# Optimization experiments

Hardware: AMD Instinct MI355X
Metric: run time of the kernel (lower is better)

The kernel has to match this reference:

```python
import jax, jax.numpy as jnp
import numpy as np

N = 50000
E = 800000
IN_C, HID, OUT_C = 128, 128, 40
EPS = 1e-5  # BatchNorm eps


def setup_inputs() -> dict:
    key = jax.random.key(0)
    ks = jax.random.split(key, 8)
    x = jax.random.normal(ks[0], (N, IN_C), dtype=jnp.float32)
    edge_index = jax.random.randint(ks[1], (2, E), 0, N, dtype=jnp.int64)
    s1 = 1.0 / np.sqrt(IN_C)
    s2 = 1.0 / np.sqrt(HID)
    return {
        "x": x,
        "edge_index": edge_index,
        "W1": jax.random.uniform(ks[2], (IN_C, HID), jnp.float32, -s1, s1),
        "b1": jnp.zeros((HID,), jnp.float32),
        "g1": jnp.ones((HID,), jnp.float32),
        "beta1": jnp.zeros((HID,), jnp.float32),
        "W2": jax.random.uniform(ks[3], (HID, HID), jnp.float32, -s2, s2),
        "b2": jnp.zeros((HID,), jnp.float32),
        "g2": jnp.ones((HID,), jnp.float32),
        "beta2": jnp.zeros((HID,), jnp.float32),
        "W3": jax.random.uniform(ks[4], (HID, OUT_C), jnp.float32, -s2, s2),
        "b3": jnp.zeros((OUT_C,), jnp.float32),
    }


def _gcn_norm(src, dst, num_nodes):
    # symmetric normalization D^-1/2 A D^-1/2, no self loops, unit edge weights
    deg = jax.ops.segment_sum(jnp.ones_like(dst, dtype=jnp.float32), dst,
                              num_segments=num_nodes)
    dinv = jnp.where(deg > 0, jax.lax.rsqrt(jnp.maximum(deg, 1.0)), 0.0)
    return dinv[src] * dinv[dst]  # [E]


def _conv(h, W, b, src, dst, norm, num_nodes):
    h = h @ W  # linear transform first (fewer message features)
    msg = norm[:, None] * h[src]  # [E, F] gather
    out = jax.ops.segment_sum(msg, dst, num_segments=num_nodes)  # scatter-add
    return out + b


def _bn_relu(h, g, beta):
    mu = jnp.mean(h, axis=0)
    var = jnp.mean(jnp.square(h - mu), axis=0)  # biased, as torch BN
    hn = (h - mu) * jax.lax.rsqrt(var + EPS) * g + beta
    return jax.nn.relu(hn)


def reference(x, edge_index, W1, b1, g1, beta1, W2, b2, g2, beta2, W3, b3):
    src, dst = edge_index[0], edge_index[1]
    norm = _gcn_norm(src, dst, N)  # cached=True: shared across layers
    h = _bn_relu(_conv(x, W1, b1, src, dst, norm, N), g1, beta1)
    h = _bn_relu(_conv(h, W2, b2, src, dst, norm, N), g2, beta2)
    return _conv(h, W3, b3, src, dst, norm, N)
```

## Files before the change

kernel.cpp:

```cpp
#include <hip/hip_runtime.h>
#include <hip/hip_fp16.h>

typedef _Float16 half8 __attribute__((ext_vector_type(8)));
typedef float floatx4 __attribute__((ext_vector_type(4)));


__device__ __forceinline__ void unpack8(uint4 v, float* f) {
    const __half2* hp = (const __half2*)&v;
    float2 a = __half22float2(hp[0]);
    float2 b = __half22float2(hp[1]);
    float2 c = __half22float2(hp[2]);
    float2 d = __half22float2(hp[3]);
    f[0] = a.x; f[1] = a.y; f[2] = b.x; f[3] = b.y;
    f[4] = c.x; f[5] = c.y; f[6] = d.x; f[7] = d.y;
}

__device__ __forceinline__ uint4 pack8(const float* f) {
    __half2 h0 = __floats2half2_rn(f[0], f[1]);
    __half2 h1 = __floats2half2_rn(f[2], f[3]);
    __half2 h2 = __floats2half2_rn(f[4], f[5]);
    __half2 h3 = __floats2half2_rn(f[6], f[7]);
    uint4 v;
    v.x = *(const unsigned int*)&h0;
    v.y = *(const unsigned int*)&h1;
    v.z = *(const unsigned int*)&h2;
    v.w = *(const unsigned int*)&h3;
    return v;
}


__global__ void k_setup(const float* __restrict__ W1, const float* __restrict__ W2,
                        const float* __restrict__ W3, __half* __restrict__ Wt1,
                        __half* __restrict__ Wt2, __half* __restrict__ Wt3,
                        int* __restrict__ zp, int zn) {
    const int PW = 2 * 128 * 128 + 48 * 128;
    int i = blockIdx.x * 256 + threadIdx.x;
    if (i < 128 * 128) {
        int n = i >> 7, k = i & 127;
        Wt1[i] = __float2half(W1[(size_t)k * 128 + n]);
    } else if (i < 2 * 128 * 128) {
        int j = i - 128 * 128;
        int n = j >> 7, k = j & 127;
        Wt2[j] = __float2half(W2[(size_t)k * 128 + n]);
    } else if (i < PW) {
        int j = i - 2 * 128 * 128;
        int n = j >> 7, k = j & 127;
        Wt3[j] = (n < 40) ? __float2half(W3[(size_t)k * 40 + n]) : __half(0.f);
    } else {
        int j = i - PW;
        if (j < zn) zp[j] = 0;
    }
}


__global__ void k_deg_xcd(const int* __restrict__ dst, int* __restrict__ deg,
                          int E, int rs) {
    int lo = (blockIdx.x & 7) * rs;
    int i = (blockIdx.x >> 3) * 256 + threadIdx.x;
    if (i < E) {
        int d = dst[i];
        if (d >= lo && d < lo + rs) atomicAdd(&deg[d], 1);
    }
}

__global__ void k_place_xcd(const int* __restrict__ src, const int* __restrict__ dst,
                            int* __restrict__ cursor, unsigned short* __restrict__ sidx,
                            int E, int rs) {
    int lo = (blockIdx.x & 7) * rs;
    int i = (blockIdx.x >> 3) * 256 + threadIdx.x;
    if (i < E) {
        int d = dst[i];
        if (d >= lo && d < lo + rs) {
            int pos = atomicAdd(&cursor[d], 1);
            sidx[pos] = (unsigned short)src[i];
        }
    }
}

__global__ __launch_bounds__(256) void k_chunkscan(const int* __restrict__ deg,
                                                   int* __restrict__ bsum, int n) {
    __shared__ int ls[256];
    int t = threadIdx.x;
    int s = 0;
    int base = t * 256;
    for (int k = 0; k < 256; ++k) {
        int idx = base + k;
        if (idx < n) s += deg[idx];
    }
    ls[t] = s;
    __syncthreads();
    for (int off = 1; off < 256; off <<= 1) {
        int v = t >= off ? ls[t - off] : 0;
        __syncthreads();
        ls[t] += v;
        __syncthreads();
    }
    bsum[t] = ls[t] - s;
}

__global__ void k_scanchunk(const int* __restrict__ cnt, const int* __restrict__ bsum,
                            int* __restrict__ row_ptr, int* __restrict__ cursor,
                            float* __restrict__ dinv, int n, int E) {
    __shared__ int ls[256];
    int i = blockIdx.x * 256 + threadIdx.x;
    int v = i < n ? cnt[i] : 0;
    ls[threadIdx.x] = v;
    __syncthreads();
    for (int off = 1; off < 256; off <<= 1) {
        int t = threadIdx.x >= off ? ls[threadIdx.x - off] : 0;
        __syncthreads();
        ls[threadIdx.x] += t;
        __syncthreads();
    }
    if (i < n) {
        int ex = ls[threadIdx.x] - v + bsum[blockIdx.x];
        row_ptr[i] = ex;
        cursor[i] = ex;
        dinv[i] = v > 0 ? rsqrtf((float)v) : 0.f;
    }
    if (i == n - 1) row_ptr[n] = E;
}


template <int CT, int STRIDE, int VALID, int AMODE, int CSPLIT>
__global__ __launch_bounds__(256) void k_gemm_mfma(const void* __restrict__ Ap,
                                                   const __half* __restrict__ Wt,
                                                   const float* __restrict__ sums32,
                                                   const float* __restrict__ sumsq32,
                                                   const float* __restrict__ g,
                                                   const float* __restrict__ beta,
                                                   const float* __restrict__ dinv,
                                                   __half* __restrict__ C, int nrows) {
    constexpr int CW = CT * 16;
    __shared__ char lw[CT * 16 * 256];
    __shared__ float lsc[128], lsh[128];
    const int rowblk = (CSPLIT == 2) ? (blockIdx.x >> 1) : blockIdx.x;
    const int colblk = (CSPLIT == 2) ? (blockIdx.x & 1) : 0;

    const int lane = threadIdx.x & 63;
    const int wid = threadIdx.x >> 6;
    const int l15 = lane & 15;
    const int lg = lane >> 4;
    const int rowbase = rowblk * 128 + wid * 32;

    uint4 raw16[2][4];
    float4 raw32[2][4][2];
#pragma unroll
    for (int r = 0; r < 2; ++r) {
        int row = rowbase + r * 16 + l15;
        bool ok = row < nrows;
#pragma unroll
        for (int kk = 0; kk < 4; ++kk) {
            const int c0 = kk * 32 + lg * 8;
            if (AMODE == 0) {
                const float* a = (const float*)Ap + (size_t)row * 128 + c0;
                raw32[r][kk][0] = ok ? *(const float4*)a : make_float4(0.f, 0.f, 0.f, 0.f);
                raw32[r][kk][1] = ok ? *(const float4*)(a + 4) : make_float4(0.f, 0.f, 0.f, 0.f);
            } else {
                raw16[r][kk] = ok ? *(const uint4*)((const __half*)Ap + (size_t)row * 128 + c0)
                                  : make_uint4(0, 0, 0, 0);
            }
        }
    }

    const int nu4 = CT * 16 * 16;
    for (int i = threadIdx.x; i < nu4; i += 256) {
        int row = i >> 4, k8 = i & 15;
        uint4 v = ((const uint4*)Wt)[(colblk * CW + row) * 16 + k8];
        *(uint4*)(lw + ((row * 256 + k8 * 16) ^ ((row & 7) << 4))) = v;
    }
    if (AMODE == 1 && threadIdx.x < 128) {
        int c = threadIdx.x;
        float s = 0.f, q = 0.f;
        for (int k2 = 0; k2 < 32; ++k2) {
            s += sums32[k2 * 128 + c];
            q += sumsq32[k2 * 128 + c];
        }
        float inv_n = 1.f / (float)nrows;
        float mu = s * inv_n;
        float var = q * inv_n - mu * mu;
        float rs = rsqrtf(var + 1e-5f);
        float sc = rs * g[c];
        lsc[c] = sc;
        lsh[c] = beta[c] - mu * sc;
    }
    __syncthreads();

    half8 a2[2][4];
#pragma unroll
    for (int r = 0; r < 2; ++r) {
#pragma unroll
        for (int kk = 0; kk < 4; ++kk) {
            const int c0 = kk * 32 + lg * 8;
            half8 h;
            if (AMODE == 0) {
                float4 v0 = raw32[r][kk][0];
                float4 v1 = raw32[r][kk][1];
                h[0] = (_Float16)v0.x; h[1] = (_Float16)v0.y;
                h[2] = (_Float16)v0.z; h[3] = (_Float16)v0.w;
                h[4] = (_Float16)v1.x; h[5] = (_Float16)v1.y;
                h[6] = (_Float16)v1.z; h[7] = (_Float16)v1.w;
            } else {
                float f[8];
                unpack8(raw16[r][kk], f);
                float4 s0 = *(const float4*)&lsc[c0];
                float4 s1 = *(const float4*)&lsc[c0 + 4];
                float4 t0 = *(const float4*)&lsh[c0];
                float4 t1 = *(const float4*)&lsh[c0 + 4];
                h[0] = (_Float16)fmaxf(f[0] * s0.x + t0.x, 0.f);
                h[1] = (_Float16)fmaxf(f[1] * s0.y + t0.y, 0.f);
                h[2] = (_Float16)fmaxf(f[2] * s0.z + t0.z, 0.f);
                h[3] = (_Float16)fmaxf(f[3] * s0.w + t0.w, 0.f);
                h[4] = (_Float16)fmaxf(f[4] * s1.x + t1.x, 0.f);
                h[5] = (_Float16)fmaxf(f[5] * s1.y + t1.y, 0.f);
                h[6] = (_Float16)fmaxf(f[6] * s1.z + t1.z, 0.f);
                h[7] = (_Float16)fmaxf(f[7] * s1.w + t1.w, 0.f);
            }
            a2[r][kk] = h;
        }
    }

    floatx4 acc[2][CT];
#pragma unroll
    for (int r = 0; r < 2; ++r)
#pragma unroll
        for (int c = 0; c < CT; ++c) acc[r][c] = (floatx4){0.f, 0.f, 0.f, 0.f};

#pragma unroll
    for (int kk = 0; kk < 4; ++kk) {
#pragma unroll
        for (int c = 0; c < CT; ++c) {
            int wrow = c * 16 + l15;
            half8 bfrag = *(const half8*)(lw + ((wrow * 256 + kk * 64 + lg * 16) ^ ((wrow & 7) << 4)));
#pragma unroll
            for (int r = 0; r < 2; ++r)
                acc[r][c] = __builtin_amdgcn_mfma_f32_16x16x32_f16(a2[r][kk], bfrag, acc[r][c], 0, 0, 0);
        }
    }

    const int BV = (VALID - colblk * CW) < CW ? (VALID - colblk * CW) : CW;
    __syncthreads();
    __half* ct = (__half*)lw;
#pragma unroll
    for (int r = 0; r < 2; ++r) {
        int lr0 = wid * 32 + r * 16 + lg * 4;
        float d4[4];
#pragma unroll
        for (int j = 0; j < 4; ++j) {
            int row = rowblk * 128 + lr0 + j;
            d4[j] = row < nrows ? dinv[row] : 0.f;
        }
#pragma unroll
        for (int c = 0; c < CT; ++c) {
            int col = c * 16 + l15;
#pragma unroll
            for (int j = 0; j < 4; ++j) {
                int lrow = lr0 + j;
                int cc = (CW == 64) ? (col ^ (((lrow >> 2) & 1) << 5)) : col;
                ct[lrow * CW + cc] = __float2half(acc[r][c][j] * d4[j]);
            }
        }
    }
    __syncthreads();
    constexpr int U = CW / 8;
    for (int i = threadIdx.x; i < 128 * U; i += 256) {
        int lrow = i / U, u = i % U;
        int row = rowblk * 128 + lrow;
        int col0 = u * 8;
        if (row < nrows && col0 < BV) {
            int cc = (CW == 64) ? (col0 ^ (((lrow >> 2) & 1) << 5)) : col0;
            uint4 v = *(const uint4*)&ct[lrow * CW + cc];
            *(uint4*)(&C[(size_t)row * STRIDE + colblk * CW + col0]) = v;
        }
    }
}


__global__ __launch_bounds__(256) void k_agg128_stats(const __half* __restrict__ M,
                                                      const int* __restrict__ rp,
                                                      const unsigned short* __restrict__ sidx,
                                                      const float* __restrict__ dinv,
                                                      __half* __restrict__ Hout,
                                                      float* __restrict__ sums32,
                                                      float* __restrict__ sumsq32, int n) {
    int d = blockIdx.x * 16 + (threadIdx.x >> 4);
    int lane = threadIdx.x & 15;
    float acc[8] = {0.f, 0.f, 0.f, 0.f, 0.f, 0.f, 0.f, 0.f};
    if (d < n) {
        int beg = rp[d], end = rp[d + 1];
        int j = beg;
        for (; j + 8 <= end; j += 8) {
            uint4 v[8];
#pragma unroll
            for (int t = 0; t < 8; ++t)
                v[t] = *(const uint4*)(M + (size_t)sidx[j + t] * 128 + lane * 8);
#pragma unroll
            for (int t = 0; t < 8; ++t) {
                float f[8];
                unpack8(v[t], f);
#pragma unroll
                for (int i = 0; i < 8; ++i) acc[i] += f[i];
            }
        }
        for (; j + 4 <= end; j += 4) {
            uint4 v[4];
#pragma unroll
            for (int t = 0; t < 4; ++t)
                v[t] = *(const uint4*)(M + (size_t)sidx[j + t] * 128 + lane * 8);
#pragma unroll
            for (int t = 0; t < 4; ++t) {
                float f[8];
                unpack8(v[t], f);
#pragma unroll
                for (int i = 0; i < 8; ++i) acc[i] += f[i];
            }
        }
        for (; j < end; ++j) {
            uint4 v = *(const uint4*)(M + (size_t)sidx[j] * 128 + lane * 8);
            float f[8];
            unpack8(v, f);
#pragma unroll
            for (int i = 0; i < 8; ++i) acc[i] += f[i];
        }
        float sc = dinv[d];
#pragma unroll
        for (int i = 0; i < 8; ++i) acc[i] *= sc;
        *(uint4*)(Hout + (size_t)d * 128 + lane * 8) = pack8(acc);
    }
    float sq[8];
#pragma unroll
    for (int i = 0; i < 8; ++i) sq[i] = acc[i] * acc[i];
#pragma unroll
    for (int m = 16; m <= 32; m <<= 1) {
#pragma unroll
        for (int i = 0; i < 8; ++i) {
            acc[i] += __shfl_xor(acc[i], m);
            sq[i]  += __shfl_xor(sq[i], m);
        }
    }
    __shared__ float lsw[2][4][16][8];
    int wid = threadIdx.x >> 6, wl = threadIdx.x & 63;
    if (wl < 16) {
#pragma unroll
        for (int i = 0; i < 8; ++i) {
            lsw[0][wid][wl][i] = acc[i];
            lsw[1][wid][wl][i] = sq[i];
        }
    }
    __syncthreads();
    if (threadIdx.x < 128) {
        int c = threadIdx.x;
        int lc = c >> 3, e = c & 7;
        float ss = 0.f, qq = 0.f;
#pragma unroll
        for (int w = 0; w < 4; ++w) {
            ss += lsw[0][w][lc][e];
            qq += lsw[1][w][lc][e];
        }
        int sh = (blockIdx.x & 31) * 128;
        atomicAdd(&sums32[sh + c], ss);
        atomicAdd(&sumsq32[sh + c], qq);
    }
}


__global__ void k_agg40_f16(const __half* __restrict__ M,
                            const int* __restrict__ rp,
                            const unsigned short* __restrict__ sidx,
                            const float* __restrict__ dinv,
                            const float* __restrict__ b3,
                            float* __restrict__ out, int n) {
    int i = blockIdx.x * 256 + threadIdx.x;
    if (i >= n * 5) return;
    int d = i / 5, q = i % 5;
    int beg = rp[d], end = rp[d + 1];
    float acc[8] = {0.f, 0.f, 0.f, 0.f, 0.f, 0.f, 0.f, 0.f};
    int j = beg;
    for (; j + 4 <= end; j += 4) {
        uint4 v0 = *(const uint4*)(M + (size_t)sidx[j] * 64 + q * 8);
        uint4 v1 = *(const uint4*)(M + (size_t)sidx[j + 1] * 64 + q * 8);
        uint4 v2 = *(const uint4*)(M + (size_t)sidx[j + 2] * 64 + q * 8);
        uint4 v3 = *(const uint4*)(M + (size_t)sidx[j + 3] * 64 + q * 8);
        float f0[8], f1[8], f2[8], f3[8];
        unpack8(v0, f0); unpack8(v1, f1); unpack8(v2, f2); unpack8(v3, f3);
#pragma unroll
        for (int k = 0; k < 8; ++k)
            acc[k] += (f0[k] + f1[k]) + (f2[k] + f3[k]);
    }
    for (; j < end; ++j) {
        uint4 v = *(const uint4*)(M + (size_t)sidx[j] * 64 + q * 8);
        float f[8];
        unpack8(v, f);
#pragma unroll
        for (int k = 0; k < 8; ++k) acc[k] += f[k];
    }
    float sc = dinv[d];
    float4 b0 = *(const float4*)&b3[q * 8];
    float4 b1 = *(const float4*)&b3[q * 8 + 4];
    float4 r0, r1;
    r0.x = acc[0] * sc + b0.x; r0.y = acc[1] * sc + b0.y;
    r0.z = acc[2] * sc + b0.z; r0.w = acc[3] * sc + b0.w;
    r1.x = acc[4] * sc + b1.x; r1.y = acc[5] * sc + b1.y;
    r1.z = acc[6] * sc + b1.z; r1.w = acc[7] * sc + b1.w;
    float* o = out + (size_t)d * 40 + q * 8;
    *(float4*)o = r0;
    *(float4*)(o + 4) = r1;
}


extern "C" void kernel_launch(void* const* d_in, const int* in_sizes, int n_in,
                              void* d_out, int out_size, void* d_ws, size_t ws_size,
                              hipStream_t stream) {
    const float* x  = (const float*)d_in[0];
    const int*   ei = (const int*)d_in[1];
    const float* W1 = (const float*)d_in[2];
    const float* g1 = (const float*)d_in[4];
    const float* be1= (const float*)d_in[5];
    const float* W2 = (const float*)d_in[6];
    const float* g2 = (const float*)d_in[8];
    const float* be2= (const float*)d_in[9];
    const float* W3 = (const float*)d_in[10];
    const float* b3 = (const float*)d_in[11];

    const int N = in_sizes[0] / 128;
    const int E = in_sizes[1] / 2;
    const int* srcv = ei;
    const int* dstv = ei + E;
    const int NB = (N + 255) / 256;
    const int RS = (N + 7) / 8;
    const int EB8 = 8 * ((E + 255) / 256);

    __half* M    = (__half*)d_ws;
    __half* Hb   = M + (size_t)N * 128;
    __half* t3   = Hb + (size_t)N * 128;
    __half* Wt1  = t3 + (size_t)N * 64;
    __half* Wt2  = Wt1 + 128 * 128;
    __half* Wt3  = Wt2 + 128 * 128;
    float* dinv    = (float*)(Wt3 + 48 * 128);
    int*   deg     = (int*)(dinv + N);
    float* sumsA   = (float*)(deg + N);
    float* sumsqA  = sumsA + 32 * 128;
    float* sumsB   = sumsqA + 32 * 128;
    float* sumsqB  = sumsB + 32 * 128;
    int*   row_ptr = (int*)(sumsqB + 32 * 128);
    int*   cursor  = row_ptr + N + 1;
    unsigned short* sidx = (unsigned short*)(cursor + N);
    int*   bsum    = (int*)(sidx + E);
    float* out     = (float*)d_out;

    const int GB = (N + 127) / 128;
    const int ZN = N + 4 * 32 * 128;
    const int SETUP_TOT = 2 * 128 * 128 + 48 * 128 + ZN;

    k_setup<<<(SETUP_TOT + 255) / 256, 256, 0, stream>>>(W1, W2, W3, Wt1, Wt2, Wt3, deg, ZN);
    k_deg_xcd<<<EB8, 256, 0, stream>>>(dstv, deg, E, RS);
    k_chunkscan<<<1, 256, 0, stream>>>(deg, bsum, N);
    k_scanchunk<<<NB, 256, 0, stream>>>(deg, bsum, row_ptr, cursor, dinv, N, E);
    k_place_xcd<<<EB8, 256, 0, stream>>>(srcv, dstv, cursor, sidx, E, RS);

    k_gemm_mfma<4, 128, 128, 0, 2><<<GB * 2, 256, 0, stream>>>(x, Wt1, nullptr, nullptr, nullptr, nullptr, dinv, M, N);
    k_agg128_stats<<<(N + 15) / 16, 256, 0, stream>>>(M, row_ptr, sidx, dinv, Hb, sumsA, sumsqA, N);

    k_gemm_mfma<4, 128, 128, 1, 2><<<GB * 2, 256, 0, stream>>>(Hb, Wt2, sumsA, sumsqA, g1, be1, dinv, M, N);
    k_agg128_stats<<<(N + 15) / 16, 256, 0, stream>>>(M, row_ptr, sidx, dinv, Hb, sumsB, sumsqB, N);

    k_gemm_mfma<3, 64, 40, 1, 1><<<GB, 256, 0, stream>>>(Hb, Wt3, sumsB, sumsqB, g2, be2, dinv, t3, N);
    k_agg40_f16<<<(N * 5 + 255) / 256, 256, 0, stream>>>(t3, row_ptr, sidx, dinv, b3, out, N);
}
```

Baseline: 229.1 us.

## Stripe feature matrices into 32-column slabs and aggregate per slab for cache locality

GEMM outputs and aggregation inputs now use a striped layout: four slabs of N×32 halves instead of row-major N×128. Aggregation runs one 32-column pass per block, with blocks interleaved so each XCD's L2 holds a smaller gather working set. Edge indices are also pre-converted to 16-bit in the setup kernel, which reduces index traffic in the degree and placement kernels. The cost is more blocks and more index reads per aggregation, plus an extra conversion pass over all edges.

```diff
diff --git a/kernel.cpp b/kernel.cpp
--- a/kernel.cpp
+++ b/kernel.cpp
@@ -32,7 +32,9 @@
 __global__ void k_setup(const float* __restrict__ W1, const float* __restrict__ W2,
                         const float* __restrict__ W3, __half* __restrict__ Wt1,
                         __half* __restrict__ Wt2, __half* __restrict__ Wt3,
-                        int* __restrict__ zp, int zn) {
+                        int* __restrict__ zp, int zn,
+                        const int* __restrict__ ei, unsigned short* __restrict__ e16,
+                        int E) {
     const int PW = 2 * 128 * 128 + 48 * 128;
     int i = blockIdx.x * 256 + threadIdx.x;
     if (i < 128 * 128) {
@@ -46,14 +48,17 @@
         int j = i - 2 * 128 * 128;
         int n = j >> 7, k = j & 127;
         Wt3[j] = (n < 40) ? __float2half(W3[(size_t)k * 40 + n]) : __half(0.f);
+    } else if (i < PW + zn) {
+        zp[i - PW] = 0;
     } else {
-        int j = i - PW;
-        if (j < zn) zp[j] = 0;
-    }
-}
-
-
-__global__ void k_deg_xcd(const int* __restrict__ dst, int* __restrict__ deg,
+        int j = i - PW - zn;
+        if (j < E) e16[j] = (unsigned short)ei[E + j];
+        else if (j < 2 * E) e16[j] = (unsigned short)ei[j - E];
+    }
+}
+
+
+__global__ void k_deg_xcd(const unsigned short* __restrict__ dst, int* __restrict__ deg,
                           int E, int rs) {
     int lo = (blockIdx.x & 7) * rs;
     int i = (blockIdx.x >> 3) * 256 + threadIdx.x;
@@ -63,7 +68,8 @@
     }
 }
 
-__global__ void k_place_xcd(const int* __restrict__ src, const int* __restrict__ dst,
+__global__ void k_place_xcd(const unsigned short* __restrict__ src,
+                            const unsigned short* __restrict__ dst,
                             int* __restrict__ cursor, unsigned short* __restrict__ sidx,
                             int E, int rs) {
     int lo = (blockIdx.x & 7) * rs;
@@ -72,7 +78,7 @@
         int d = dst[i];
         if (d >= lo && d < lo + rs) {
             int pos = atomicAdd(&cursor[d], 1);
-            sidx[pos] = (unsigned short)src[i];
+            sidx[pos] = src[i];
         }
     }
 }
@@ -122,7 +128,7 @@
 }
 
 
-template <int CT, int STRIDE, int VALID, int AMODE, int CSPLIT>
+template <int CT, int STRIDE, int VALID, int AMODE, int CSPLIT, int ASTRIPE, int CSTRIPE>
 __global__ __launch_bounds__(256) void k_gemm_mfma(const void* __restrict__ Ap,
                                                    const __half* __restrict__ Wt,
                                                    const float* __restrict__ sums32,
@@ -156,6 +162,9 @@
                 const float* a = (const float*)Ap + (size_t)row * 128 + c0;
                 raw32[r][kk][0] = ok ? *(const float4*)a : make_float4(0.f, 0.f, 0.f, 0.f);
                 raw32[r][kk][1] = ok ? *(const float4*)(a + 4) : make_float4(0.f, 0.f, 0.f, 0.f);
+            } else if (ASTRIPE) {
+                const __half* a = (const __half*)Ap + ((size_t)kk * nrows + row) * 32 + lg * 8;
+                raw16[r][kk] = ok ? *(const uint4*)a : make_uint4(0, 0, 0, 0);
             } else {
                 raw16[r][kk] = ok ? *(const uint4*)((const __half*)Ap + (size_t)row * 128 + c0)
                                   : make_uint4(0, 0, 0, 0);
@@ -238,7 +247,6 @@
         }
     }
 
-    const int BV = (VALID - colblk * CW) < CW ? (VALID - colblk * CW) : CW;
     __syncthreads();
     __half* ct = (__half*)lw;
 #pragma unroll
@@ -267,56 +275,51 @@
         int lrow = i / U, u = i % U;
         int row = rowblk * 128 + lrow;
         int col0 = u * 8;
-        if (row < nrows && col0 < BV) {
+        int g2 = colblk * CW + col0;
+        if (row < nrows && (CSTRIPE || col0 < VALID)) {
             int cc = (CW == 64) ? (col0 ^ (((lrow >> 2) & 1) << 5)) : col0;
             uint4 v = *(const uint4*)&ct[lrow * CW + cc];
-            *(uint4*)(&C[(size_t)row * STRIDE + colblk * CW + col0]) = v;
-        }
-    }
-}
-
-
-__global__ __launch_bounds__(256) void k_agg128_stats(const __half* __restrict__ M,
-                                                      const int* __restrict__ rp,
-                                                      const unsigned short* __restrict__ sidx,
-                                                      const float* __restrict__ dinv,
-                                                      __half* __restrict__ Hout,
-                                                      float* __restrict__ sums32,
-                                                      float* __restrict__ sumsq32, int n) {
-    int d = blockIdx.x * 16 + (threadIdx.x >> 4);
-    int lane = threadIdx.x & 15;
+            if (CSTRIPE)
+                *(uint4*)(&C[((size_t)(g2 >> 5) * nrows + row) * 32 + (g2 & 31)]) = v;
+            else
+                *(uint4*)(&C[(size_t)row * STRIDE + g2]) = v;
+        }
+    }
+}
+
+
+__global__ __launch_bounds__(256) void k_agg32_stats(const __half* __restrict__ M4,
+                                                     const int* __restrict__ rp,
+                                                     const unsigned short* __restrict__ sidx,
+                                                     const float* __restrict__ dinv,
+                                                     __half* __restrict__ H4,
+                                                     float* __restrict__ sums32,
+                                                     float* __restrict__ sumsq32, int n) {
+    int b = blockIdx.x;
+    int pass = (b >> 1) & 3;
+    int nodeblk = (b >> 3) * 2 + (b & 1);
+    int tid = threadIdx.x;
+    int d = nodeblk * 64 + (tid >> 2);
+    int lane4 = tid & 3;
+    const __half* Mp = M4 + (size_t)pass * n * 32;
+
     float acc[8] = {0.f, 0.f, 0.f, 0.f, 0.f, 0.f, 0.f, 0.f};
     if (d < n) {
         int beg = rp[d], end = rp[d + 1];
         int j = beg;
-        for (; j + 8 <= end; j += 8) {
-            uint4 v[8];
-#pragma unroll
-            for (int t = 0; t < 8; ++t)
-                v[t] = *(const uint4*)(M + (size_t)sidx[j + t] * 128 + lane * 8);
-#pragma unroll
-            for (int t = 0; t < 8; ++t) {
-                float f[8];
-                unpack8(v[t], f);
-#pragma unroll
-                for (int i = 0; i < 8; ++i) acc[i] += f[i];
-            }
-        }
         for (; j + 4 <= end; j += 4) {
-            uint4 v[4];
-#pragma unroll
-            for (int t = 0; t < 4; ++t)
-                v[t] = *(const uint4*)(M + (size_t)sidx[j + t] * 128 + lane * 8);
-#pragma unroll
-            for (int t = 0; t < 4; ++t) {
-                float f[8];
-                unpack8(v[t], f);
-#pragma unroll
-                for (int i = 0; i < 8; ++i) acc[i] += f[i];
-            }
+            uint4 v0 = *(const uint4*)(Mp + (size_t)sidx[j]     * 32 + lane4 * 8);
+            uint4 v1 = *(const uint4*)(Mp + (size_t)sidx[j + 1] * 32 + lane4 * 8);
+            uint4 v2 = *(const uint4*)(Mp + (size_t)sidx[j + 2] * 32 + lane4 * 8);
+            uint4 v3 = *(const uint4*)(Mp + (size_t)sidx[j + 3] * 32 + lane4 * 8);
+            float f0[8], f1[8], f2[8], f3[8];
+            unpack8(v0, f0); unpack8(v1, f1); unpack8(v2, f2); unpack8(v3, f3);
+#pragma unroll
+            for (int i = 0; i < 8; ++i)
+                acc[i] += (f0[i] + f1[i]) + (f2[i] + f3[i]);
         }
         for (; j < end; ++j) {
-            uint4 v = *(const uint4*)(M + (size_t)sidx[j] * 128 + lane * 8);
+            uint4 v = *(const uint4*)(Mp + (size_t)sidx[j] * 32 + lane4 * 8);
             float f[8];
             unpack8(v, f);
 #pragma unroll
@@ -325,22 +328,23 @@
         float sc = dinv[d];
 #pragma unroll
         for (int i = 0; i < 8; ++i) acc[i] *= sc;
-        *(uint4*)(Hout + (size_t)d * 128 + lane * 8) = pack8(acc);
-    }
+        *(uint4*)(H4 + (size_t)pass * n * 32 + (size_t)d * 32 + lane4 * 8) = pack8(acc);
+    }
+
     float sq[8];
 #pragma unroll
     for (int i = 0; i < 8; ++i) sq[i] = acc[i] * acc[i];
 #pragma unroll
-    for (int m = 16; m <= 32; m <<= 1) {
+    for (int m = 4; m <= 32; m <<= 1) {
 #pragma unroll
         for (int i = 0; i < 8; ++i) {
             acc[i] += __shfl_xor(acc[i], m);
             sq[i]  += __shfl_xor(sq[i], m);
         }
     }
-    __shared__ float lsw[2][4][16][8];
-    int wid = threadIdx.x >> 6, wl = threadIdx.x & 63;
-    if (wl < 16) {
+    __shared__ float lsw[2][4][4][8];
+    int wid = tid >> 6, wl = tid & 63;
+    if (wl < 4) {
 #pragma unroll
         for (int i = 0; i < 8; ++i) {
             lsw[0][wid][wl][i] = acc[i];
@@ -348,16 +352,16 @@
         }
     }
     __syncthreads();
-    if (threadIdx.x < 128) {
-        int c = threadIdx.x;
-        int lc = c >> 3, e = c & 7;
+    if (tid < 32) {
+        int lc = tid >> 3, e = tid & 7;
         float ss = 0.f, qq = 0.f;
 #pragma unroll
         for (int w = 0; w < 4; ++w) {
             ss += lsw[0][w][lc][e];
             qq += lsw[1][w][lc][e];
         }
-        int sh = (blockIdx.x & 31) * 128;
+        int sh = (b & 31) * 128;
+        int c = pass * 32 + tid;
         atomicAdd(&sums32[sh + c], ss);
         atomicAdd(&sumsq32[sh + c], qq);
     }
@@ -424,8 +428,6 @@
 
     const int N = in_sizes[0] / 128;
     const int E = in_sizes[1] / 2;
-    const int* srcv = ei;
-    const int* dstv = ei + E;
     const int NB = (N + 255) / 256;
     const int RS = (N + 7) / 8;
     const int EB8 = 8 * ((E + 255) / 256);
@@ -445,25 +447,35 @@
     int*   row_ptr = (int*)(sumsqB + 32 * 128);
     int*   cursor  = row_ptr + N + 1;
     unsigned short* sidx = (unsigned short*)(cursor + N);
-    int*   bsum    = (int*)(sidx + E);
+    unsigned short* e16  = sidx + E;
+    int*   bsum    = (int*)(e16 + 2 * E);
     float* out     = (float*)d_out;
+
+    const unsigned short* dst16 = e16;
+    const unsigned short* src16 = e16 + E;
 
     const int GB = (N + 127) / 128;
     const int ZN = N + 4 * 32 * 128;
-    const int SETUP_TOT = 2 * 128 * 128 + 48 * 128 + ZN;
-
-    k_setup<<<(SETUP_TOT + 255) / 256, 256, 0, stream>>>(W1, W2, W3, Wt1, Wt2, Wt3, deg, ZN);
-    k_deg_xcd<<<EB8, 256, 0, stream>>>(dstv, deg, E, RS);
+    const int SETUP_TOT = 2 * 128 * 128 + 48 * 128 + ZN + 2 * E;
+    const int NB64 = (N + 63) / 64;
+    const int AGG_GRID = 8 * ((NB64 + 1) / 2);
+
+    k_setup<<<(SETUP_TOT + 255) / 256, 256, 0, stream>>>(W1, W2, W3, Wt1, Wt2, Wt3,
+                                                         deg, ZN, ei, e16, E);
+    k_deg_xcd<<<EB8, 256, 0, stream>>>(dst16, deg, E, RS);
     k_chunkscan<<<1, 256, 0, stream>>>(deg, bsum, N);
     k_scanchunk<<<NB, 256, 0, stream>>>(deg, bsum, row_ptr, cursor, dinv, N, E);
-    k_place_xcd<<<EB8, 256, 0, stream>>>(srcv, dstv, cursor, sidx, E, RS);
-
-    k_gemm_mfma<4, 128, 128, 0, 2><<<GB * 2, 256, 0, stream>>>(x, Wt1, nullptr, nullptr, nullptr, nullptr, dinv, M, N);
-    k_agg128_stats<<<(N + 15) / 16, 256, 0, stream>>>(M, row_ptr, sidx, dinv, Hb, sumsA, sumsqA, N);
-
-    k_gemm_mfma<4, 128, 128, 1, 2><<<GB * 2, 256, 0, stream>>>(Hb, Wt2, sumsA, sumsqA, g1, be1, dinv, M, N);
-    k_agg128_stats<<<(N + 15) / 16, 256, 0, stream>>>(M, row_ptr, sidx, dinv, Hb, sumsB, sumsqB, N);
-
-    k_gemm_mfma<3, 64, 40, 1, 1><<<GB, 256, 0, stream>>>(Hb, Wt3, sumsB, sumsqB, g2, be2, dinv, t3, N);
+    k_place_xcd<<<EB8, 256, 0, stream>>>(src16, dst16, cursor, sidx, E, RS);
+
+    k_gemm_mfma<4, 128, 128, 0, 2, 0, 1><<<GB * 2, 256, 0, stream>>>(
+        x, Wt1, nullptr, nullptr, nullptr, nullptr, dinv, M, N);
+    k_agg32_stats<<<AGG_GRID, 256, 0, stream>>>(M, row_ptr, sidx, dinv, Hb, sumsA, sumsqA, N);
+
+    k_gemm_mfma<4, 128, 128, 1, 2, 1, 1><<<GB * 2, 256, 0, stream>>>(
+        Hb, Wt2, sumsA, sumsqA, g1, be1, dinv, M, N);
+    k_agg32_stats<<<AGG_GRID, 256, 0, stream>>>(M, row_ptr, sidx, dinv, Hb, sumsB, sumsqB, N);
+
+    k_gemm_mfma<3, 64, 40, 1, 1, 1, 0><<<GB, 256, 0, stream>>>(
+        Hb, Wt3, sumsB, sumsqB, g2, be2, dinv, t3, N);
     k_agg40_f16<<<(N * 5 + 255) / 256, 256, 0, stream>>>(t3, row_ptr, sidx, dinv, b3, out, N);
 }
```

Result: faster. 221.3 us, median of 2 (-3.4%).
